# Performance work log

Measured on AMD Instinct MI355X. Metric: run time of the kernel, lower is better.

The kernel has to match this reference:

```python
import jax, jax.numpy as jnp
import numpy as np

VOCAB, H, E, B, S = 50257, 1024, 1024, 64, 2048


def setup_inputs() -> dict:
    key = jax.random.key(0)
    ks = jax.random.split(key, 12)
    s = 0.02
    return {
        "input_seq": jax.random.randint(ks[0], (B,), 0, VOCAB),
        "last_hidden": jax.random.normal(ks[1], (1, B, H), jnp.float32),
        "last_cell": jax.random.normal(ks[2], (1, B, H), jnp.float32),
        "encoder_outputs": jax.random.normal(ks[3], (S, B, H), jnp.float32),
        "emb_W": jax.random.normal(ks[4], (VOCAB, E), jnp.float32) * s,
        "W_ih": jax.random.normal(ks[5], (4 * H, E), jnp.float32) * s,
        "W_hh": jax.random.normal(ks[6], (4 * H, H), jnp.float32) * s,
        "b_ih": jnp.zeros((4 * H,), jnp.float32),
        "b_hh": jnp.zeros((4 * H,), jnp.float32),
        "concat_W": jax.random.normal(ks[7], (H, 2 * H), jnp.float32) * s,
        "concat_b": jnp.zeros((H,), jnp.float32),
        "out_W": jax.random.normal(ks[8], (VOCAB, H), jnp.float32) * s,
        "out_b": jnp.zeros((VOCAB,), jnp.float32),
    }


def reference(input_seq, last_hidden, last_cell, encoder_outputs,
              emb_W, W_ih, W_hh, b_ih, b_hh,
              concat_W, concat_b, out_W, out_b):
    # Embedding lookup (dropout is identity in eval mode)
    x = emb_W[input_seq]                      # [B, E]
    h0 = last_hidden[0]                       # [B, H]
    c0 = last_cell[0]                         # [B, H]
    # Single LSTM step (PyTorch gate order: i, f, g, o)
    gates = x @ W_ih.T + b_ih + h0 @ W_hh.T + b_hh   # [B, 4H]
    i, f, g, o = jnp.split(gates, 4, axis=-1)
    c = jax.nn.sigmoid(f) * c0 + jax.nn.sigmoid(i) * jnp.tanh(g)
    h = jax.nn.sigmoid(o) * jnp.tanh(c)       # [B, H] == rnn_output
    # 'dot' attention: energies[b, s] = h[b] . enc[s, b]  (vectorized)
    energies = jnp.einsum('bh,sbh->bs', h, encoder_outputs)   # [B, S]
    attn = jax.nn.softmax(energies, axis=1)                   # [B, S]
    context = jnp.einsum('bs,sbh->bh', attn, encoder_outputs) # [B, H]
    concat_out = jnp.tanh(jnp.concatenate([h, context], axis=1) @ concat_W.T + concat_b)
    output = concat_out @ out_W.T + out_b                     # [B, VOCAB]
    return output, h[None], c[None], attn[:, None, :]
```

## Files before the change

### kernel.cpp

```cpp
#include <hip/hip_runtime.h>
#include <hip/hip_bf16.h>
#include <math.h>

#define BB 64
#define HH 1024
#define SS 2048
#define VV 50257

typedef float f32x4 __attribute__((ext_vector_type(4)));
typedef short bf16x8 __attribute__((ext_vector_type(8)));

__device__ __forceinline__ float sigf(float x){ return 1.0f/(1.0f+__expf(-x)); }
__device__ __forceinline__ short f2bf(float f){
  __hip_bfloat16 h = __float2bfloat16(f);
  return __builtin_bit_cast(short, h);
}
__device__ __forceinline__ float bf2f(short s){
  __hip_bfloat16 h = __builtin_bit_cast(__hip_bfloat16, s);
  return __bfloat162float(h);
}

__global__ void k_prep(const int* __restrict__ seq, const float* __restrict__ embW,
                       const float* __restrict__ h0,
                       short* __restrict__ Ahi, short* __restrict__ Alo){
  const int b = blockIdx.x;
  const int k = threadIdx.x * 8;
  const float* src = (k < 1024) ? (embW + (size_t)seq[b]*1024 + k)
                                : (h0 + (size_t)b*1024 + (k - 1024));
  float4 v0 = *(const float4*)src;
  float4 v1 = *(const float4*)(src + 4);
  float v[8] = {v0.x,v0.y,v0.z,v0.w,v1.x,v1.y,v1.z,v1.w};
  bf16x8 hi, lo;
  #pragma unroll
  for (int j = 0; j < 8; ++j) {
    short h = f2bf(v[j]);
    hi[j] = h;
    lo[j] = f2bf(v[j] - bf2f(h));
  }
  *(bf16x8*)(Ahi + (size_t)b*2048 + k) = hi;
  *(bf16x8*)(Alo + (size_t)b*2048 + k) = lo;
}

__global__ __launch_bounds__(256, 3)
void k_gates(const short* __restrict__ Ahi, const short* __restrict__ Alo,
             const float* __restrict__ W_ih, const float* __restrict__ W_hh,
             float* __restrict__ dst)
{
  const int tid = threadIdx.x;
  const int wave = tid >> 6, lane = tid & 63;
  const int r = lane & 15, g = lane >> 4;
  const int nb = blockIdx.x, sk = blockIdx.y;
  const int n0 = nb*128 + wave*32;
  const int kbase = sk*128;
  const float* Wm = (kbase < 1024) ? W_ih : W_hh;
  const int kw = (kbase < 1024) ? kbase : (kbase - 1024);

  f32x4 acc[4][2] = {};

  #pragma unroll
  for (int ks = 0; ks < 4; ++ks) {
    const int kk = kbase + ks*32 + g*8;
    const int ko = kw   + ks*32 + g*8;
    bf16x8 ahi[4], alo[4];
    #pragma unroll
    for (int mf = 0; mf < 4; ++mf) {
      ahi[mf] = *(const bf16x8*)(Ahi + (size_t)(mf*16 + r)*2048 + kk);
      alo[mf] = *(const bf16x8*)(Alo + (size_t)(mf*16 + r)*2048 + kk);
    }
    #pragma unroll
    for (int nf = 0; nf < 2; ++nf) {
      const int n = n0 + nf*16 + r;
      const float* wp = Wm + (size_t)n*1024 + ko;
      float4 w0 = *(const float4*)wp;
      float4 w1 = *(const float4*)(wp + 4);
      float wv[8] = {w0.x,w0.y,w0.z,w0.w,w1.x,w1.y,w1.z,w1.w};
      bf16x8 whi, wlo;
      #pragma unroll
      for (int j = 0; j < 8; ++j) {
        short h = f2bf(wv[j]);
        whi[j] = h;
        wlo[j] = f2bf(wv[j] - bf2f(h));
      }
      #pragma unroll
      for (int mf = 0; mf < 4; ++mf) {
        acc[mf][nf] = __builtin_amdgcn_mfma_f32_16x16x32_bf16(ahi[mf], whi, acc[mf][nf], 0,0,0);
        acc[mf][nf] = __builtin_amdgcn_mfma_f32_16x16x32_bf16(alo[mf], whi, acc[mf][nf], 0,0,0);
        acc[mf][nf] = __builtin_amdgcn_mfma_f32_16x16x32_bf16(ahi[mf], wlo, acc[mf][nf], 0,0,0);
      }
    }
  }

  #pragma unroll
  for (int nf = 0; nf < 2; ++nf) {
    const int n = n0 + nf*16 + r;
    #pragma unroll
    for (int mf = 0; mf < 4; ++mf)
      #pragma unroll
      for (int j = 0; j < 4; ++j)
        dst[((size_t)sk*64 + (mf*16 + g*4 + j))*4096 + n] = acc[mf][nf][j];
  }
}

__global__ void k_rlstm(const float* __restrict__ part, const float* __restrict__ b_ih,
                        const float* __restrict__ b_hh, const float* __restrict__ c0,
                        float* __restrict__ h_out, float* __restrict__ c_out,
                        short* __restrict__ concA, int SK){
  int idx = blockIdx.x*256 + threadIdx.x;
  int b = idx >> 10, k = idx & 1023;
  float gi = b_ih[k]      + b_hh[k];
  float gf = b_ih[1024+k] + b_hh[1024+k];
  float gg = b_ih[2048+k] + b_hh[2048+k];
  float go = b_ih[3072+k] + b_hh[3072+k];
  const float* p = part + (size_t)b*4096 + k;
  for (int s = 0; s < SK; ++s) {
    const float* ps = p + (size_t)s*64*4096;
    gi += ps[0]; gf += ps[1024]; gg += ps[2048]; go += ps[3072];
  }
  float c = sigf(gf)*c0[idx] + sigf(gi)*tanhf(gg);
  float h = sigf(go)*tanhf(c);
  c_out[idx] = c;
  h_out[idx] = h;
  concA[(size_t)b*2048 + k] = f2bf(h);
}

__global__ __launch_bounds__(256)
void k_mfma(const short* __restrict__ A, int lda,
            const float* __restrict__ W1, int ldw,
            float* __restrict__ dst, int N, int Ktot)
{
  const int tid  = threadIdx.x;
  const int wave = tid >> 6, lane = tid & 63;
  const int nb = blockIdx.x, sk = blockIdx.y, SK = gridDim.y;
  const int ksteps = Ktot >> 5;
  const int kps = ksteps / SK;
  const int k0 = sk * kps;
  const int n0 = nb*128 + wave*32;
  const int r = lane & 15, g = lane >> 4;

  f32x4 acc[4][2] = {};

  for (int ks = k0; ks < k0 + kps; ++ks) {
    const int kk = (ks << 5) + g*8;
    bf16x8 af[4];
    #pragma unroll
    for (int mf = 0; mf < 4; ++mf)
      af[mf] = *(const bf16x8*)(A + (size_t)(mf*16 + r)*lda + kk);
    #pragma unroll
    for (int nf = 0; nf < 2; ++nf) {
      const int n = n0 + nf*16 + r;
      const float* wp = W1 + (size_t)n*ldw + kk;
      float4 w0 = *(const float4*)wp;
      float4 w1 = *(const float4*)(wp + 4);
      bf16x8 bfr;
      bfr[0]=f2bf(w0.x); bfr[1]=f2bf(w0.y); bfr[2]=f2bf(w0.z); bfr[3]=f2bf(w0.w);
      bfr[4]=f2bf(w1.x); bfr[5]=f2bf(w1.y); bfr[6]=f2bf(w1.z); bfr[7]=f2bf(w1.w);
      #pragma unroll
      for (int mf = 0; mf < 4; ++mf)
        acc[mf][nf] = __builtin_amdgcn_mfma_f32_16x16x32_bf16(af[mf], bfr, acc[mf][nf], 0, 0, 0);
    }
  }

  #pragma unroll
  for (int nf = 0; nf < 2; ++nf) {
    const int n = n0 + nf*16 + r;
    #pragma unroll
    for (int mf = 0; mf < 4; ++mf)
      #pragma unroll
      for (int j = 0; j < 4; ++j)
        dst[((size_t)sk*64 + (mf*16 + g*4 + j))*N + n] = acc[mf][nf][j];
  }
}

__global__ void k_reduce(const float* __restrict__ part, const float* __restrict__ bias,
                         short* __restrict__ dstb, int N, int SK){
  size_t idx = (size_t)blockIdx.x*256 + threadIdx.x;
  if (idx >= (size_t)64*N) return;
  int b = (int)(idx / N), n = (int)(idx % N);
  float v = bias[n];
  for (int s = 0; s < SK; ++s) v += part[((size_t)s*64 + b)*N + n];
  dstb[(size_t)b*N + n] = f2bf(tanhf(v));
}

__global__ __launch_bounds__(256)
void k_logits3(const short* __restrict__ A, const float* __restrict__ W,
               const float* __restrict__ bias, float* __restrict__ out)
{
  __shared__ short Wl[64 * 256];
  const int tid = threadIdx.x;
  const int wave = tid >> 6, lane = tid & 63;
  const int r = lane & 15, g = lane >> 4;
  const int n0 = blockIdx.x * 64;
  const int myrow = wave*16 + r;

#define LOADC(CC, ST) { _Pragma("unroll") \
    for (int rr = 0; rr < 16; ++rr) { \
      const int row = wave*16 + rr; \
      const int grow = (n0 + row < VV) ? (n0 + row) : (VV - 1); \
      ST[rr] = *(const float4*)(W + (size_t)grow*1024 + (CC)*256 + lane*4); \
    } }
#define WRITEC(ST) { _Pragma("unroll") \
    for (int rr = 0; rr < 16; ++rr) { \
      const int row = wave*16 + rr; \
      short4 s4; \
      s4.x = f2bf(ST[rr].x); s4.y = f2bf(ST[rr].y); \
      s4.z = f2bf(ST[rr].z); s4.w = f2bf(ST[rr].w); \
      *(short4*)((char*)Wl + ((row*512 + lane*8) ^ ((row&7)<<4))) = s4; \
    } }

  f32x4 acc[4] = {};
  {
    float4 st[16];
    LOADC(0, st);
    WRITEC(st);
  }
  __syncthreads();

  for (int c = 0; c < 4; ++c) {
    float4 st2[16];
    if (c < 3) LOADC(c+1, st2);
    const int kc = c*256;
    #pragma unroll 4
    for (int ks = 0; ks < 8; ++ks) {
      const bf16x8 bfr = *(const bf16x8*)((char*)Wl +
            ((myrow*512 + ks*64 + g*16) ^ ((myrow&7)<<4)));
      const int kk = kc + ks*32 + g*8;
      #pragma unroll
      for (int mf = 0; mf < 4; ++mf) {
        const bf16x8 af = *(const bf16x8*)(A + (size_t)(mf*16 + r)*1024 + kk);
        acc[mf] = __builtin_amdgcn_mfma_f32_16x16x32_bf16(af, bfr, acc[mf], 0, 0, 0);
      }
    }
    __syncthreads();
    if (c < 3) {
      WRITEC(st2);
      __syncthreads();
    }
  }
#undef LOADC
#undef WRITEC

  const int n = n0 + wave*16 + r;
  if (n < VV) {
    const float bv = bias[n];
    #pragma unroll
    for (int mf = 0; mf < 4; ++mf)
      #pragma unroll
      for (int j = 0; j < 4; ++j)
        out[(size_t)(mf*16 + g*4 + j)*VV + n] = acc[mf][j] + bv;
  }
}

__global__ __launch_bounds__(256)
void k_attn_part(const float* __restrict__ h, const float* __restrict__ enc,
                 float* __restrict__ energ, float* __restrict__ mpart,
                 float* __restrict__ lpart, float* __restrict__ ctxpart, int C){
  const int b  = blockIdx.x & 63;
  const int ch = blockIdx.x >> 6;
  const int wave = threadIdx.x >> 6;
  const int lane = threadIdx.x & 63;
  const int rows = SS / C;
  const int rpw  = rows >> 2;
  const int sw = ch*rows + wave*rpw;

  float4 hq0, hq1, hq2, hq3;
  {
    const float* hb = h + (size_t)b*HH + lane*4;
    hq0 = *(const float4*)(hb);
    hq1 = *(const float4*)(hb + 256);
    hq2 = *(const float4*)(hb + 512);
    hq3 = *(const float4*)(hb + 768);
  }
  float m = -INFINITY, l = 0.f;
  float cacc[16];
  #pragma unroll
  for (int j = 0; j < 16; ++j) cacc[j] = 0.f;

  for (int i = 0; i < rpw; i += 2) {
    const float* ep = enc + ((size_t)(sw+i)*BB + b)*HH + lane*4;
    const float* fp = ep + (size_t)BB*HH;
    const float4 e0 = *(const float4*)(ep);
    const float4 e1 = *(const float4*)(ep + 256);
    const float4 e2 = *(const float4*)(ep + 512);
    const float4 e3 = *(const float4*)(ep + 768);
    const float4 f0 = *(const float4*)(fp);
    const float4 f1 = *(const float4*)(fp + 256);
    const float4 f2 = *(const float4*)(fp + 512);
    const float4 f3 = *(const float4*)(fp + 768);
    float p = hq0.x*e0.x + hq0.y*e0.y + hq0.z*e0.z + hq0.w*e0.w
            + hq1.x*e1.x + hq1.y*e1.y + hq1.z*e1.z + hq1.w*e1.w
            + hq2.x*e2.x + hq2.y*e2.y + hq2.z*e2.z + hq2.w*e2.w
            + hq3.x*e3.x + hq3.y*e3.y + hq3.z*e3.z + hq3.w*e3.w;
    float q = hq0.x*f0.x + hq0.y*f0.y + hq0.z*f0.z + hq0.w*f0.w
            + hq1.x*f1.x + hq1.y*f1.y + hq1.z*f1.z + hq1.w*f1.w
            + hq2.x*f2.x + hq2.y*f2.y + hq2.z*f2.z + hq2.w*f2.w
            + hq3.x*f3.x + hq3.y*f3.y + hq3.z*f3.z + hq3.w*f3.w;
    p += __shfl_xor(p, 1);  q += __shfl_xor(q, 1);
    p += __shfl_xor(p, 2);  q += __shfl_xor(q, 2);
    p += __shfl_xor(p, 4);  q += __shfl_xor(q, 4);
    p += __shfl_xor(p, 8);  q += __shfl_xor(q, 8);
    p += __shfl_xor(p, 16); q += __shfl_xor(q, 16);
    p += __shfl_xor(p, 32); q += __shfl_xor(q, 32);
    if (lane == 0) {
      float2 pq; pq.x = p; pq.y = q;
      *(float2*)(energ + (size_t)b*SS + sw + i) = pq;
    }
    const float mn = fmaxf(fmaxf(m, p), q);
    const float sc = __expf(m - mn);
    const float pe = __expf(p - mn);
    const float qe = __expf(q - mn);
    l = l*sc + pe + qe;
    cacc[0]  = cacc[0]*sc  + pe*e0.x + qe*f0.x;
    cacc[1]  = cacc[1]*sc  + pe*e0.y + qe*f0.y;
    cacc[2]  = cacc[2]*sc  + pe*e0.z + qe*f0.z;
    cacc[3]  = cacc[3]*sc  + pe*e0.w + qe*f0.w;
    cacc[4]  = cacc[4]*sc  + pe*e1.x + qe*f1.x;
    cacc[5]  = cacc[5]*sc  + pe*e1.y + qe*f1.y;
    cacc[6]  = cacc[6]*sc  + pe*e1.z + qe*f1.z;
    cacc[7]  = cacc[7]*sc  + pe*e1.w + qe*f1.w;
    cacc[8]  = cacc[8]*sc  + pe*e2.x + qe*f2.x;
    cacc[9]  = cacc[9]*sc  + pe*e2.y + qe*f2.y;
    cacc[10] = cacc[10]*sc + pe*e2.z + qe*f2.z;
    cacc[11] = cacc[11]*sc + pe*e2.w + qe*f2.w;
    cacc[12] = cacc[12]*sc + pe*e3.x + qe*f3.x;
    cacc[13] = cacc[13]*sc + pe*e3.y + qe*f3.y;
    cacc[14] = cacc[14]*sc + pe*e3.z + qe*f3.z;
    cacc[15] = cacc[15]*sc + pe*e3.w + qe*f3.w;
    m = mn;
  }

  __shared__ float sm[4], sl[4];
  __shared__ float sctx[4][1024];
  if (lane == 0) { sm[wave] = m; sl[wave] = l; }
  __syncthreads();
  const float mg = fmaxf(fmaxf(sm[0], sm[1]), fmaxf(sm[2], sm[3]));
  const float lg = sl[0]*__expf(sm[0]-mg) + sl[1]*__expf(sm[1]-mg)
                 + sl[2]*__expf(sm[2]-mg) + sl[3]*__expf(sm[3]-mg);
  const float scw = __expf(m - mg);
  #pragma unroll
  for (int j = 0; j < 4; ++j) {
    float4 v;
    v.x = cacc[j*4+0]*scw; v.y = cacc[j*4+1]*scw;
    v.z = cacc[j*4+2]*scw; v.w = cacc[j*4+3]*scw;
    *(float4*)&sctx[wave][j*256 + lane*4] = v;
  }
  __syncthreads();
  const int d = threadIdx.x * 4;
  const float4 a0 = *(const float4*)&sctx[0][d];
  const float4 a1 = *(const float4*)&sctx[1][d];
  const float4 a2 = *(const float4*)&sctx[2][d];
  const float4 a3 = *(const float4*)&sctx[3][d];
  float4 rr;
  rr.x = a0.x+a1.x+a2.x+a3.x; rr.y = a0.y+a1.y+a2.y+a3.y;
  rr.z = a0.z+a1.z+a2.z+a3.z; rr.w = a0.w+a1.w+a2.w+a3.w;
  *(float4*)(ctxpart + ((size_t)(b*C + ch))*HH + d) = rr;
  if (threadIdx.x == 0) { mpart[b*C+ch] = mg; lpart[b*C+ch] = lg; }
}

__global__ void k_attn_fin(const float* __restrict__ mpart, const float* __restrict__ lpart,
                           const float* __restrict__ ctxpart, const float* __restrict__ energ,
                           float* __restrict__ attn, short* __restrict__ concA, int C){
  const int b = blockIdx.x, tid = threadIdx.x;
  float m = -INFINITY;
  for (int c = 0; c < C; ++c) m = fmaxf(m, mpart[b*C+c]);
  float l = 0.f;
  for (int c = 0; c < C; ++c) l += lpart[b*C+c] * __expf(mpart[b*C+c] - m);
  const float inv = 1.0f / l;
  float ax = 0.f, ay = 0.f, az = 0.f, aw = 0.f;
  for (int c = 0; c < C; ++c) {
    const float w = __expf(mpart[b*C+c] - m);
    const float* cp = ctxpart + ((size_t)(b*C+c))*HH + tid*4;
    ax += w*cp[0]; ay += w*cp[1]; az += w*cp[2]; aw += w*cp[3];
  }
  ax *= inv; ay *= inv; az *= inv; aw *= inv;
  short* ca = concA + (size_t)b*2048 + 1024 + tid*4;
  ca[0] = f2bf(ax); ca[1] = f2bf(ay); ca[2] = f2bf(az); ca[3] = f2bf(aw);
  for (int j = 0; j < 8; ++j) {
    const int s = j*256 + tid;
    attn[(size_t)b*SS + s] = __expf(energ[(size_t)b*SS + s] - m) * inv;
  }
}

extern "C" void kernel_launch(void* const* d_in, const int* in_sizes, int n_in,
                              void* d_out, int out_size, void* d_ws, size_t ws_size,
                              hipStream_t stream){
  const int*   seq  = (const int*)  d_in[0];
  const float* h0   = (const float*)d_in[1];
  const float* c0   = (const float*)d_in[2];
  const float* enc  = (const float*)d_in[3];
  const float* embW = (const float*)d_in[4];
  const float* W_ih = (const float*)d_in[5];
  const float* W_hh = (const float*)d_in[6];
  const float* b_ih = (const float*)d_in[7];
  const float* b_hh = (const float*)d_in[8];
  const float* cW   = (const float*)d_in[9];
  const float* cb   = (const float*)d_in[10];
  const float* oW   = (const float*)d_in[11];
  const float* ob   = (const float*)d_in[12];
  float* out = (float*)d_out;

  float* ws = (float*)d_ws;
  const size_t o_energ = 0;
  const size_t o_concA = 131072;
  const size_t o_concB = 196608;
  const size_t o_Ahi   = 229376;
  const size_t o_Alo   = 294912;
  const size_t o_mp    = 360448;
  const size_t SKPART  = 4194304;
  int C = 32;
  for (;;) {
    size_t need = (o_mp + (size_t)64*C*2 + (size_t)64*C*1024 + SKPART) * sizeof(float);
    if (need <= ws_size || C == 1) break;
    C >>= 1;
  }
  float* energ   = ws + o_energ;
  short* concA   = (short*)(ws + o_concA);
  short* concB   = (short*)(ws + o_concB);
  short* Ahi     = (short*)(ws + o_Ahi);
  short* Alo     = (short*)(ws + o_Alo);
  float* mpart   = ws + o_mp;
  float* lpart   = mpart + (size_t)64*C;
  float* ctxpart = lpart + (size_t)64*C;
  float* skpart  = ctxpart + (size_t)64*C*1024;

  const size_t o_h = 3216448, o_c = 3281984, o_attn = 3347520;

  k_prep<<<64, 256, 0, stream>>>(seq, embW, h0, Ahi, Alo);
  k_gates<<<dim3(32,16), 256, 0, stream>>>(Ahi, Alo, W_ih, W_hh, skpart);
  k_rlstm<<<256, 256, 0, stream>>>(skpart, b_ih, b_hh, c0, out + o_h, out + o_c,
                                   concA, 16);
  k_attn_part<<<64*C, 256, 0, stream>>>(out + o_h, enc, energ, mpart, lpart, ctxpart, C);
  k_attn_fin<<<64, 256, 0, stream>>>(mpart, lpart, ctxpart, energ, out + o_attn, concA, C);
  k_mfma<<<dim3(8,16), 256, 0, stream>>>(concA, 2048, cW, 2048, skpart, 1024, 2048);
  k_reduce<<<256, 256, 0, stream>>>(skpart, cb, concB, 1024, 16);
  k_logits3<<<786, 256, 0, stream>>>(concB, oW, ob, out);
}
```

Before: 294.8 us.

## Split logits GEMM over K across waves, load weights directly into registers

The output-projection kernel no longer stages fp32 weights into shared memory and loops sequentially over K. Each block now covers 32 vocab columns, and each of its 4 waves takes one 256-wide K slice. Weights are read straight from global memory into bf16 MFMA fragments, and the partial sums are combined through a shared-memory reduction. This is meant to raise the block count (1571 instead of 786) and the number of memory requests in flight for the bandwidth-bound 200MB weight read. The cost is an extra LDS reduction, and each block now reads the activation matrix once per 32 columns instead of once per 64.

Result: faster. 262.6 us (-10.9%).

```diff
diff --git a/kernel.cpp b/kernel.cpp
--- a/kernel.cpp
+++ b/kernel.cpp
@@ -182,71 +182,63 @@
 }
 
 __global__ __launch_bounds__(256)
-void k_logits3(const short* __restrict__ A, const float* __restrict__ W,
+void k_logits4(const short* __restrict__ A, const float* __restrict__ W,
                const float* __restrict__ bias, float* __restrict__ out)
 {
-  __shared__ short Wl[64 * 256];
+  __shared__ float red[4][32][64];
   const int tid = threadIdx.x;
   const int wave = tid >> 6, lane = tid & 63;
   const int r = lane & 15, g = lane >> 4;
-  const int n0 = blockIdx.x * 64;
-  const int myrow = wave*16 + r;
-
-#define LOADC(CC, ST) { _Pragma("unroll") \
-    for (int rr = 0; rr < 16; ++rr) { \
-      const int row = wave*16 + rr; \
-      const int grow = (n0 + row < VV) ? (n0 + row) : (VV - 1); \
-      ST[rr] = *(const float4*)(W + (size_t)grow*1024 + (CC)*256 + lane*4); \
-    } }
-#define WRITEC(ST) { _Pragma("unroll") \
-    for (int rr = 0; rr < 16; ++rr) { \
-      const int row = wave*16 + rr; \
-      short4 s4; \
-      s4.x = f2bf(ST[rr].x); s4.y = f2bf(ST[rr].y); \
-      s4.z = f2bf(ST[rr].z); s4.w = f2bf(ST[rr].w); \
-      *(short4*)((char*)Wl + ((row*512 + lane*8) ^ ((row&7)<<4))) = s4; \
-    } }
-
-  f32x4 acc[4] = {};
-  {
-    float4 st[16];
-    LOADC(0, st);
-    WRITEC(st);
-  }
+  const int n0 = blockIdx.x * 32;
+  const int nA = n0 + r, nB = n0 + 16 + r;
+  const int nAc = (nA < VV) ? nA : (VV - 1);
+  const int nBc = (nB < VV) ? nB : (VV - 1);
+  const int kb = wave * 256;
+
+  const short* A0 = A + (size_t)r*1024 + kb + g*8;
+  const float* wA = W + (size_t)nAc*1024 + kb + g*8;
+  const float* wB = W + (size_t)nBc*1024 + kb + g*8;
+
+  f32x4 acc[4][2] = {};
+
+  #pragma unroll
+  for (int ks = 0; ks < 8; ++ks) {
+    const int o = ks*32;
+    const float4 u0 = *(const float4*)(wA + o);
+    const float4 u1 = *(const float4*)(wA + o + 4);
+    const float4 v0 = *(const float4*)(wB + o);
+    const float4 v1 = *(const float4*)(wB + o + 4);
+    bf16x8 bA, bB;
+    bA[0]=f2bf(u0.x); bA[1]=f2bf(u0.y); bA[2]=f2bf(u0.z); bA[3]=f2bf(u0.w);
+    bA[4]=f2bf(u1.x); bA[5]=f2bf(u1.y); bA[6]=f2bf(u1.z); bA[7]=f2bf(u1.w);
+    bB[0]=f2bf(v0.x); bB[1]=f2bf(v0.y); bB[2]=f2bf(v0.z); bB[3]=f2bf(v0.w);
+    bB[4]=f2bf(v1.x); bB[5]=f2bf(v1.y); bB[6]=f2bf(v1.z); bB[7]=f2bf(v1.w);
+    #pragma unroll
+    for (int mf = 0; mf < 4; ++mf) {
+      const bf16x8 af = *(const bf16x8*)(A0 + (size_t)mf*16*1024 + o);
+      acc[mf][0] = __builtin_amdgcn_mfma_f32_16x16x32_bf16(af, bA, acc[mf][0], 0,0,0);
+      acc[mf][1] = __builtin_amdgcn_mfma_f32_16x16x32_bf16(af, bB, acc[mf][1], 0,0,0);
+    }
+  }
+
+  #pragma unroll
+  for (int nf = 0; nf < 2; ++nf)
+    #pragma unroll
+    for (int mf = 0; mf < 4; ++mf)
+      #pragma unroll
+      for (int j = 0; j < 4; ++j)
+        red[wave][nf*16 + mf*4 + j][lane] = acc[mf][nf][j];
   __syncthreads();
 
-  for (int c = 0; c < 4; ++c) {
-    float4 st2[16];
-    if (c < 3) LOADC(c+1, st2);
-    const int kc = c*256;
-    #pragma unroll 4
-    for (int ks = 0; ks < 8; ++ks) {
-      const bf16x8 bfr = *(const bf16x8*)((char*)Wl +
-            ((myrow*512 + ks*64 + g*16) ^ ((myrow&7)<<4)));
-      const int kk = kc + ks*32 + g*8;
-      #pragma unroll
-      for (int mf = 0; mf < 4; ++mf) {
-        const bf16x8 af = *(const bf16x8*)(A + (size_t)(mf*16 + r)*1024 + kk);
-        acc[mf] = __builtin_amdgcn_mfma_f32_16x16x32_bf16(af, bfr, acc[mf], 0, 0, 0);
-      }
-    }
-    __syncthreads();
-    if (c < 3) {
-      WRITEC(st2);
-      __syncthreads();
-    }
-  }
-#undef LOADC
-#undef WRITEC
-
-  const int n = n0 + wave*16 + r;
-  if (n < VV) {
-    const float bv = bias[n];
-    #pragma unroll
-    for (int mf = 0; mf < 4; ++mf)
-      #pragma unroll
-      for (int j = 0; j < 4; ++j)
-        out[(size_t)(mf*16 + g*4 + j)*VV + n] = acc[mf][j] + bv;
+  #pragma unroll
+  for (int vi = 0; vi < 8; ++vi) {
+    const int v  = wave*8 + vi;
+    const int nf = v >> 4, mf = (v >> 2) & 3, j = v & 3;
+    const float s = red[0][v][lane] + red[1][v][lane]
+                  + red[2][v][lane] + red[3][v][lane];
+    const int col = n0 + nf*16 + r;
+    if (col < VV)
+      out[(size_t)(mf*16 + g*4 + j)*VV + col] = s + bias[col];
   }
 }
 
@@ -432,5 +424,5 @@
   k_attn_fin<<<64, 256, 0, stream>>>(mpart, lpart, ctxpart, energ, out + o_attn, concA, C);
   k_mfma<<<dim3(8,16), 256, 0, stream>>>(concA, 2048, cW, 2048, skpart, 1024, 2048);
   k_reduce<<<256, 256, 0, stream>>>(skpart, cb, concB, 1024, 16);
-  k_logits3<<<786, 256, 0, stream>>>(concB, oW, ob, out);
-}
+  k_logits4<<<1571, 256, 0, stream>>>(concB, oW, ob, out);
+}
```
